# Kernel optimization log

Hardware: AMD Instinct MI355X
Metric: run time of the kernel (lower is better)

The kernel has to match this reference:

```python
import jax, jax.numpy as jnp
import numpy as np

N, D = 8192, 1024
NUM_CLASSES = 128
PPC = 4  # prototypes per class
P = NUM_CLASSES * PPC
ALPHA = 1.0
EPS = 1e-9


def setup_inputs() -> dict:
    key = jax.random.key(0)
    k1, k2, k3 = jax.random.split(key, 3)
    x = jax.random.normal(k1, (N, D), dtype=jnp.float32)
    y = jax.random.randint(k2, (N,), 0, NUM_CLASSES, dtype=jnp.int64)
    prototypes = jax.random.normal(k3, (P, D), dtype=jnp.float32)
    return {"x": x, "y": y, "t_value": 1, "prototypes": prototypes}


def reference(x, y, t_value, prototypes):
    # prototype labels: i // PPC
    proto_labels = jnp.arange(P, dtype=y.dtype) // PPC  # [P]

    x_sq = jnp.sum(x * x, axis=1, keepdims=True)          # [N,1]
    p_sq = jnp.sum(prototypes * prototypes, axis=1)       # [P]
    dist = x_sq + p_sq[None, :] - 2.0 * (x @ prototypes.T)  # [N,P]

    correct_mask = proto_labels[None, :] == y[:, None]    # [N,P]
    inf = jnp.array(jnp.inf, dtype=dist.dtype)
    d1 = jnp.min(jnp.where(correct_mask, dist, inf), axis=1)   # [N]
    d2 = jnp.min(jnp.where(correct_mask, inf, dist), axis=1)   # [N]

    mu = (d1 - d2) / (d1 + d2 + EPS)
    alpha = jnp.log(1.0 + jnp.asarray(t_value, dtype=dist.dtype)) / ALPHA
    return jnp.mean(jax.nn.sigmoid(alpha * mu))
```

## Files before the change

kernel.cpp:

```cpp
#include <hip/hip_runtime.h>
#include <hip/hip_bf16.h>
#include <math.h>
#include <stdint.h>

#define NS 8192
#define DD 1024
#define NP 512
#define NPARTS 8
#define EPSF 1e-9f
#define BIGF 3.0e38f

typedef __attribute__((ext_vector_type(8))) short bf16x8;
typedef __attribute__((ext_vector_type(4))) float f32x4;

__device__ inline unsigned short f32_to_bf16(float f) {
    uint32_t u = __builtin_bit_cast(uint32_t, f);
    uint32_t r = (u + 0x7FFFu + ((u >> 16) & 1u)) >> 16;
    return (unsigned short)r;
}

__global__ __launch_bounds__(256) void prep_kernel(
    const float* __restrict__ x, const float* __restrict__ protos,
    unsigned short* __restrict__ xb, unsigned short* __restrict__ pb,
    float* __restrict__ xsq, float* __restrict__ psq)
{
    int row = blockIdx.x;
    const float* src;
    unsigned short* dstb;
    float* dsts;
    if (row < NS) {
        src = x + (size_t)row * DD; dstb = xb + (size_t)row * DD; dsts = xsq + row;
    } else {
        int r = row - NS;
        src = protos + (size_t)r * DD; dstb = pb + (size_t)r * DD; dsts = psq + r;
    }
    int t = threadIdx.x;
    float4 v = ((const float4*)src)[t];
    float ss = v.x * v.x + v.y * v.y + v.z * v.z + v.w * v.w;
    ushort4 o;
    o.x = f32_to_bf16(v.x); o.y = f32_to_bf16(v.y);
    o.z = f32_to_bf16(v.z); o.w = f32_to_bf16(v.w);
    ((ushort4*)dstb)[t] = o;
    for (int off = 32; off; off >>= 1) ss += __shfl_down(ss, off);
    __shared__ float red[4];
    if ((t & 63) == 0) red[t >> 6] = ss;
    __syncthreads();
    if (t == 0) dsts[0] = red[0] + red[1] + red[2] + red[3];
}

__global__ __launch_bounds__(256) void glvq_gemm(
    const unsigned short* __restrict__ Xb, const unsigned short* __restrict__ Pb,
    const float* __restrict__ xsq, const float* __restrict__ psq,
    const int* __restrict__ y,
    float* __restrict__ d1p, float* __restrict__ d2p)
{
    __shared__ unsigned short As[2][64 * 64];
    __shared__ unsigned short Bs[2][128 * 64];

    const int tid  = threadIdx.x;
    const int lane = tid & 63;
    const int wid  = tid >> 6;
    const int wr = wid >> 1, wc = wid & 1;

    const int d    = blockIdx.x;
    const int xcd  = d & 7;
    const int slot = d >> 3;
    const int mb   = xcd * 16 + (slot & 15);
    const int nb   = slot >> 4;
    const int m0   = mb * 64;
    const int n0   = nb * 128;

    const int srow   = lane >> 3;
    const int scol16 = (lane & 7) ^ srow;
    const int sub = lane & 15, g = lane >> 4;

    f32x4 acc[2][4] = {};

    auto stage = [&](int buf, int kt) {
        const int k0 = kt * 64;
#pragma unroll
        for (int j = 0; j < 2; ++j) {
            const int c = wid * 2 + j;
            const unsigned short* ga = Xb + (size_t)(m0 + c * 8 + srow) * DD + k0 + scol16 * 8;
            __builtin_amdgcn_global_load_lds(
                (const __attribute__((address_space(1))) void*)ga,
                (__attribute__((address_space(3))) void*)((char*)&As[buf][0] + c * 1024), 16, 0, 0);
        }
#pragma unroll
        for (int j = 0; j < 4; ++j) {
            const int c = wid * 4 + j;
            const unsigned short* gb = Pb + (size_t)(n0 + c * 8 + srow) * DD + k0 + scol16 * 8;
            __builtin_amdgcn_global_load_lds(
                (const __attribute__((address_space(1))) void*)gb,
                (__attribute__((address_space(3))) void*)((char*)&Bs[buf][0] + c * 1024), 16, 0, 0);
        }
    };

    auto compute = [&](int buf) {
#pragma unroll
        for (int kk = 0; kk < 2; ++kk) {
            bf16x8 a[2], b[4];
#pragma unroll
            for (int m = 0; m < 2; ++m) {
                const int row = wr * 32 + m * 16 + sub;
                const int c16 = (kk * 4 + g) ^ (row & 7);
                a[m] = *(const bf16x8*)((const char*)&As[buf][0] + row * 128 + c16 * 16);
            }
#pragma unroll
            for (int n = 0; n < 4; ++n) {
                const int row = wc * 64 + n * 16 + sub;
                const int c16 = (kk * 4 + g) ^ (row & 7);
                b[n] = *(const bf16x8*)((const char*)&Bs[buf][0] + row * 128 + c16 * 16);
            }
#pragma unroll
            for (int m = 0; m < 2; ++m)
#pragma unroll
                for (int n = 0; n < 4; ++n)
                    acc[m][n] = __builtin_amdgcn_mfma_f32_16x16x32_bf16(a[m], b[n], acc[m][n], 0, 0, 0);
        }
    };

    stage(0, 0);
    __syncthreads();
    int cur = 0;
#pragma unroll 1
    for (int kt = 0; kt < DD / 64 - 1; ++kt) {
        stage(cur ^ 1, kt + 1);
        compute(cur);
        __syncthreads();
        cur ^= 1;
    }
    compute(cur);

    float psqv[4];
    int   lab[4];
#pragma unroll
    for (int n = 0; n < 4; ++n) {
        const int col = n0 + wc * 64 + n * 16 + sub;
        psqv[n] = psq[col];
        lab[n]  = col >> 2;
    }
    const int part = nb * 2 + wc;
#pragma unroll
    for (int m = 0; m < 2; ++m) {
#pragma unroll
        for (int r = 0; r < 4; ++r) {
            const int row = m0 + wr * 32 + m * 16 + g * 4 + r;
            const float xs = xsq[row];
            const int yy = y[row];
            float d1 = BIGF, d2 = BIGF;
#pragma unroll
            for (int n = 0; n < 4; ++n) {
                const float dist = xs + psqv[n] - 2.0f * acc[m][n][r];
                if (lab[n] == yy) d1 = fminf(d1, dist);
                else              d2 = fminf(d2, dist);
            }
            for (int off = 8; off; off >>= 1) {
                d1 = fminf(d1, __shfl_xor(d1, off));
                d2 = fminf(d2, __shfl_xor(d2, off));
            }
            if (sub == 0) {
                d1p[part * NS + row] = d1;
                d2p[part * NS + row] = d2;
            }
        }
    }
}

__global__ __launch_bounds__(256) void finalize_kernel(
    const float* __restrict__ d1p, const float* __restrict__ d2p,
    const int* __restrict__ tval, float* __restrict__ bsum)
{
    const int row = blockIdx.x * 256 + threadIdx.x;
    float d1 = BIGF, d2 = BIGF;
#pragma unroll
    for (int p = 0; p < NPARTS; ++p) {
        d1 = fminf(d1, d1p[p * NS + row]);
        d2 = fminf(d2, d2p[p * NS + row]);
    }
    const float mu = (d1 - d2) / (d1 + d2 + EPSF);
    const float alpha = logf(1.0f + (float)tval[0]);
    float s = 1.0f / (1.0f + expf(-alpha * mu));
    for (int off = 32; off; off >>= 1) s += __shfl_down(s, off);
    __shared__ float red[4];
    if ((threadIdx.x & 63) == 0) red[threadIdx.x >> 6] = s;
    __syncthreads();
    if (threadIdx.x == 0) bsum[blockIdx.x] = red[0] + red[1] + red[2] + red[3];
}

__global__ void final_sum(const float* __restrict__ bsum, float* __restrict__ out) {
    float s = (threadIdx.x < NS / 256) ? bsum[threadIdx.x] : 0.0f;
    for (int off = 32; off; off >>= 1) s += __shfl_down(s, off);
    if (threadIdx.x == 0) out[0] = s * (1.0f / (float)NS);
}

extern "C" void kernel_launch(void* const* d_in, const int* in_sizes, int n_in,
                              void* d_out, int out_size, void* d_ws, size_t ws_size,
                              hipStream_t stream) {
    const float* x      = (const float*)d_in[0];
    const int*   y      = (const int*)d_in[1];
    const int*   tval   = (const int*)d_in[2];
    const float* protos = (const float*)d_in[3];
    float* out = (float*)d_out;

    char* ws = (char*)d_ws;
    unsigned short* xb  = (unsigned short*)(ws);
    unsigned short* pb  = (unsigned short*)(ws + (size_t)NS * DD * 2);
    float* xsq  = (float*)(ws + (size_t)(NS + NP) * DD * 2);
    float* psq  = (float*)(ws + (size_t)(NS + NP) * DD * 2 + NS * 4);
    float* d1p  = (float*)(ws + (size_t)(NS + NP) * DD * 2 + (NS + NP) * 4);
    float* d2p  = d1p + (size_t)NPARTS * NS;
    float* bsum = d2p + (size_t)NPARTS * NS;

    prep_kernel<<<NS + NP, 256, 0, stream>>>(x, protos, xb, pb, xsq, psq);
    glvq_gemm<<<(NS / 64) * (NP / 128), 256, 0, stream>>>(xb, pb, xsq, psq, y, d1p, d2p);
    finalize_kernel<<<NS / 256, 256, 0, stream>>>(d1p, d2p, tval, bsum);
    final_sum<<<1, 64, 0, stream>>>(bsum, out);
}
```

Baseline: 37.41 us.

## Fuse x bf16 conversion and row norms into GEMM A-tile staging

The separate pass that converts x to bf16 and computes its row squared norms is removed. The GEMM kernel now loads fp32 x directly into registers, converts it with packed bf16 conversion instructions, writes it to swizzled LDS, and accumulates the row norms along the way. The goal is to avoid writing and re-reading a 16 MB bf16 copy of x and to save a kernel launch. The cost is that each x tile is read in fp32 by all four N-blocks, which doubles A-side traffic per block, and the A loads now pass through registers instead of async global-to-LDS copies, which adds register pressure and latency to the main loop.

After: 39.59 us. 1.06x slower.

```diff
diff --git a/kernel.cpp b/kernel.cpp
--- a/kernel.cpp
+++ b/kernel.cpp
@@ -6,6 +6,9 @@
 #define NS 8192
 #define DD 1024
 #define NP 512
+#define BK 64
+#define MT 64
+#define NT 128
 #define NPARTS 8
 #define EPSF 1e-9f
 #define BIGF 3.0e38f
@@ -19,98 +22,113 @@
     return (unsigned short)r;
 }
 
-__global__ __launch_bounds__(256) void prep_kernel(
-    const float* __restrict__ x, const float* __restrict__ protos,
-    unsigned short* __restrict__ xb, unsigned short* __restrict__ pb,
-    float* __restrict__ xsq, float* __restrict__ psq)
+__device__ inline uint32_t cvt_pk(float lo, float hi) {
+    uint32_t r;
+    asm("v_cvt_pk_bf16_f32 %0, %1, %2" : "=v"(r) : "v"(lo), "v"(hi));
+    return r;
+}
+
+__global__ __launch_bounds__(256) void prep_protos(
+    const float* __restrict__ protos,
+    unsigned short* __restrict__ pb, float* __restrict__ psq)
 {
-    int row = blockIdx.x;
-    const float* src;
-    unsigned short* dstb;
-    float* dsts;
-    if (row < NS) {
-        src = x + (size_t)row * DD; dstb = xb + (size_t)row * DD; dsts = xsq + row;
-    } else {
-        int r = row - NS;
-        src = protos + (size_t)r * DD; dstb = pb + (size_t)r * DD; dsts = psq + r;
-    }
-    int t = threadIdx.x;
-    float4 v = ((const float4*)src)[t];
+    const int row = blockIdx.x;
+    const int t = threadIdx.x;
+    float4 v = ((const float4*)(protos + (size_t)row * DD))[t];
     float ss = v.x * v.x + v.y * v.y + v.z * v.z + v.w * v.w;
     ushort4 o;
     o.x = f32_to_bf16(v.x); o.y = f32_to_bf16(v.y);
     o.z = f32_to_bf16(v.z); o.w = f32_to_bf16(v.w);
-    ((ushort4*)dstb)[t] = o;
+    ((ushort4*)(pb + (size_t)row * DD))[t] = o;
     for (int off = 32; off; off >>= 1) ss += __shfl_down(ss, off);
     __shared__ float red[4];
     if ((t & 63) == 0) red[t >> 6] = ss;
     __syncthreads();
-    if (t == 0) dsts[0] = red[0] + red[1] + red[2] + red[3];
-}
-
-__global__ __launch_bounds__(256) void glvq_gemm(
-    const unsigned short* __restrict__ Xb, const unsigned short* __restrict__ Pb,
-    const float* __restrict__ xsq, const float* __restrict__ psq,
-    const int* __restrict__ y,
+    if (t == 0) psq[row] = red[0] + red[1] + red[2] + red[3];
+}
+
+__global__ __launch_bounds__(256) void glvq_fused(
+    const float* __restrict__ x, const unsigned short* __restrict__ pb,
+    const float* __restrict__ psq, const int* __restrict__ y,
     float* __restrict__ d1p, float* __restrict__ d2p)
 {
-    __shared__ unsigned short As[2][64 * 64];
-    __shared__ unsigned short Bs[2][128 * 64];
+    __shared__ unsigned short As[2][MT * BK];
+    __shared__ unsigned short Bs[2][NT * BK];
+    __shared__ float xs_l[MT];
 
     const int tid  = threadIdx.x;
     const int lane = tid & 63;
     const int wid  = tid >> 6;
-    const int wr = wid >> 1, wc = wid & 1;
-
+    const int wr = wid >> 1;
+    const int wc = wid & 1;
     const int d    = blockIdx.x;
     const int xcd  = d & 7;
     const int slot = d >> 3;
     const int mb   = xcd * 16 + (slot & 15);
     const int nb   = slot >> 4;
-    const int m0   = mb * 64;
-    const int n0   = nb * 128;
+    const int m0   = mb * MT;
+    const int n0   = nb * NT;
 
     const int srow   = lane >> 3;
     const int scol16 = (lane & 7) ^ srow;
     const int sub = lane & 15, g = lane >> 4;
 
+    const int arow = tid >> 2;
+    const int acb  = (tid & 3) * 2;
+    const float* xrow = x + (size_t)(m0 + arow) * DD;
+
     f32x4 acc[2][4] = {};
-
-    auto stage = [&](int buf, int kt) {
-        const int k0 = kt * 64;
-#pragma unroll
-        for (int j = 0; j < 2; ++j) {
-            const int c = wid * 2 + j;
-            const unsigned short* ga = Xb + (size_t)(m0 + c * 8 + srow) * DD + k0 + scol16 * 8;
-            __builtin_amdgcn_global_load_lds(
-                (const __attribute__((address_space(1))) void*)ga,
-                (__attribute__((address_space(3))) void*)((char*)&As[buf][0] + c * 1024), 16, 0, 0);
-        }
+    float xss = 0.0f;
+    float4 av[4];
+
+    auto stageB = [&](int buf, int kt) {
+        const int k0 = kt * BK;
 #pragma unroll
         for (int j = 0; j < 4; ++j) {
             const int c = wid * 4 + j;
-            const unsigned short* gb = Pb + (size_t)(n0 + c * 8 + srow) * DD + k0 + scol16 * 8;
+            const unsigned short* gb = pb + (size_t)(n0 + c * 8 + srow) * DD + k0 + scol16 * 8;
             __builtin_amdgcn_global_load_lds(
                 (const __attribute__((address_space(1))) void*)gb,
-                (__attribute__((address_space(3))) void*)((char*)&Bs[buf][0] + c * 1024), 16, 0, 0);
-        }
-    };
-
+                (__attribute__((address_space(3))) void*)((char*)&Bs[buf][0] + c * 1024),
+                16, 0, 0);
+        }
+    };
+    auto loadA = [&](int kt) {
+#pragma unroll
+        for (int j = 0; j < 2; ++j) {
+            const float* p = xrow + kt * BK + (acb + j) * 8;
+            av[2 * j]     = *(const float4*)(p);
+            av[2 * j + 1] = *(const float4*)(p + 4);
+        }
+    };
+    auto writeA = [&](int buf) {
+#pragma unroll
+        for (int j = 0; j < 2; ++j) {
+            float4 u = av[2 * j], w = av[2 * j + 1];
+            xss += u.x * u.x + u.y * u.y + u.z * u.z + u.w * u.w
+                 + w.x * w.x + w.y * w.y + w.z * w.z + w.w * w.w;
+            uint4 o;
+            o.x = cvt_pk(u.x, u.y); o.y = cvt_pk(u.z, u.w);
+            o.z = cvt_pk(w.x, w.y); o.w = cvt_pk(w.z, w.w);
+            const int c = acb + j;
+            *(uint4*)((char*)&As[buf][0] + arow * 128 + ((c ^ (arow & 7)) * 16)) = o;
+        }
+    };
     auto compute = [&](int buf) {
 #pragma unroll
         for (int kk = 0; kk < 2; ++kk) {
             bf16x8 a[2], b[4];
 #pragma unroll
             for (int m = 0; m < 2; ++m) {
-                const int row = wr * 32 + m * 16 + sub;
-                const int c16 = (kk * 4 + g) ^ (row & 7);
-                a[m] = *(const bf16x8*)((const char*)&As[buf][0] + row * 128 + c16 * 16);
+                const int rowa = wr * 32 + m * 16 + sub;
+                const int c16 = (kk * 4 + g) ^ (rowa & 7);
+                a[m] = *(const bf16x8*)((const char*)&As[buf][0] + rowa * 128 + c16 * 16);
             }
 #pragma unroll
             for (int n = 0; n < 4; ++n) {
-                const int row = wc * 64 + n * 16 + sub;
-                const int c16 = (kk * 4 + g) ^ (row & 7);
-                b[n] = *(const bf16x8*)((const char*)&Bs[buf][0] + row * 128 + c16 * 16);
+                const int rowb = wc * 64 + n * 16 + sub;
+                const int c16 = (kk * 4 + g) ^ (rowb & 7);
+                b[n] = *(const bf16x8*)((const char*)&Bs[buf][0] + rowb * 128 + c16 * 16);
             }
 #pragma unroll
             for (int m = 0; m < 2; ++m)
@@ -120,17 +138,25 @@
         }
     };
 
-    stage(0, 0);
-    __syncthreads();
+    loadA(0); stageB(0, 0); writeA(0);
+    __syncthreads();
+
     int cur = 0;
 #pragma unroll 1
-    for (int kt = 0; kt < DD / 64 - 1; ++kt) {
-        stage(cur ^ 1, kt + 1);
+    for (int kt = 0; kt < DD / BK - 1; ++kt) {
+        stageB(cur ^ 1, kt + 1);
+        loadA(kt + 1);
         compute(cur);
+        writeA(cur ^ 1);
         __syncthreads();
         cur ^= 1;
     }
     compute(cur);
+
+    xss += __shfl_xor(xss, 1);
+    xss += __shfl_xor(xss, 2);
+    if ((tid & 3) == 0) xs_l[arow] = xss;
+    __syncthreads();
 
     float psqv[4];
     int   lab[4];
@@ -145,9 +171,9 @@
     for (int m = 0; m < 2; ++m) {
 #pragma unroll
         for (int r = 0; r < 4; ++r) {
-            const int row = m0 + wr * 32 + m * 16 + g * 4 + r;
-            const float xs = xsq[row];
-            const int yy = y[row];
+            const int rl = wr * 32 + m * 16 + g * 4 + r;
+            const float xs = xs_l[rl];
+            const int yy = y[m0 + rl];
             float d1 = BIGF, d2 = BIGF;
 #pragma unroll
             for (int n = 0; n < 4; ++n) {
@@ -160,8 +186,8 @@
                 d2 = fminf(d2, __shfl_xor(d2, off));
             }
             if (sub == 0) {
-                d1p[part * NS + row] = d1;
-                d2p[part * NS + row] = d2;
+                d1p[part * NS + m0 + rl] = d1;
+                d2p[part * NS + m0 + rl] = d2;
             }
         }
     }
@@ -204,16 +230,14 @@
     float* out = (float*)d_out;
 
     char* ws = (char*)d_ws;
-    unsigned short* xb  = (unsigned short*)(ws);
-    unsigned short* pb  = (unsigned short*)(ws + (size_t)NS * DD * 2);
-    float* xsq  = (float*)(ws + (size_t)(NS + NP) * DD * 2);
-    float* psq  = (float*)(ws + (size_t)(NS + NP) * DD * 2 + NS * 4);
-    float* d1p  = (float*)(ws + (size_t)(NS + NP) * DD * 2 + (NS + NP) * 4);
+    unsigned short* pb = (unsigned short*)(ws);
+    float* psq  = (float*)(ws + (size_t)NP * DD * 2);
+    float* d1p  = psq + NP;
     float* d2p  = d1p + (size_t)NPARTS * NS;
     float* bsum = d2p + (size_t)NPARTS * NS;
 
-    prep_kernel<<<NS + NP, 256, 0, stream>>>(x, protos, xb, pb, xsq, psq);
-    glvq_gemm<<<(NS / 64) * (NP / 128), 256, 0, stream>>>(xb, pb, xsq, psq, y, d1p, d2p);
+    prep_protos<<<NP, 256, 0, stream>>>(protos, pb, psq);
+    glvq_fused<<<(NS / MT) * (NP / NT), 256, 0, stream>>>(x, pb, psq, y, d1p, d2p);
     finalize_kernel<<<NS / 256, 256, 0, stream>>>(d1p, d2p, tval, bsum);
     final_sum<<<1, 64, 0, stream>>>(bsum, out);
 }
```

## Triple-buffer GEMM K-loop with vmcnt waits, single barrier, and setprio

Applied to the files above, without the earlier changes.

Moves the bf16 GEMM main loop from double to triple buffering in LDS. It keeps two tiles in flight, waits with s_waitcnt vmcnt(6) and one raw barrier per step instead of __syncthreads after compute, and raises wave priority around the MFMA section. The aim is to hide global-to-LDS load latency better and remove one barrier wait per iteration. In exchange it uses more LDS (72KB per block), which may limit occupancy, and relies on hand-counted vmcnt correctness.

New measurement: 37.42 us. Within noise of the previous version (+0.0%).

```diff
diff --git a/kernel.cpp b/kernel.cpp
--- a/kernel.cpp
+++ b/kernel.cpp
@@ -6,6 +6,10 @@
 #define NS 8192
 #define DD 1024
 #define NP 512
+#define BK 64
+#define MT 64
+#define NT 128
+#define NSTEP (DD / BK)
 #define NPARTS 8
 #define EPSF 1e-9f
 #define BIGF 3.0e38f
@@ -48,27 +52,27 @@
     if (t == 0) dsts[0] = red[0] + red[1] + red[2] + red[3];
 }
 
-__global__ __launch_bounds__(256) void glvq_gemm(
-    const unsigned short* __restrict__ Xb, const unsigned short* __restrict__ Pb,
+__global__ __launch_bounds__(256, 2) void glvq_gemm(
+    const unsigned short* __restrict__ xb, const unsigned short* __restrict__ pb,
     const float* __restrict__ xsq, const float* __restrict__ psq,
     const int* __restrict__ y,
     float* __restrict__ d1p, float* __restrict__ d2p)
 {
-    __shared__ unsigned short As[2][64 * 64];
-    __shared__ unsigned short Bs[2][128 * 64];
+    __shared__ unsigned short As[3][MT * BK];
+    __shared__ unsigned short Bs[3][NT * BK];
 
     const int tid  = threadIdx.x;
     const int lane = tid & 63;
     const int wid  = tid >> 6;
-    const int wr = wid >> 1, wc = wid & 1;
-
+    const int wr = wid >> 1;
+    const int wc = wid & 1;
     const int d    = blockIdx.x;
     const int xcd  = d & 7;
     const int slot = d >> 3;
     const int mb   = xcd * 16 + (slot & 15);
     const int nb   = slot >> 4;
-    const int m0   = mb * 64;
-    const int n0   = nb * 128;
+    const int m0   = mb * MT;
+    const int n0   = nb * NT;
 
     const int srow   = lane >> 3;
     const int scol16 = (lane & 7) ^ srow;
@@ -77,22 +81,24 @@
     f32x4 acc[2][4] = {};
 
     auto stage = [&](int buf, int kt) {
-        const int k0 = kt * 64;
+        const int k0 = kt * BK;
 #pragma unroll
         for (int j = 0; j < 2; ++j) {
             const int c = wid * 2 + j;
-            const unsigned short* ga = Xb + (size_t)(m0 + c * 8 + srow) * DD + k0 + scol16 * 8;
+            const unsigned short* ga = xb + (size_t)(m0 + c * 8 + srow) * DD + k0 + scol16 * 8;
             __builtin_amdgcn_global_load_lds(
                 (const __attribute__((address_space(1))) void*)ga,
-                (__attribute__((address_space(3))) void*)((char*)&As[buf][0] + c * 1024), 16, 0, 0);
+                (__attribute__((address_space(3))) void*)((char*)&As[buf][0] + c * 1024),
+                16, 0, 0);
         }
 #pragma unroll
         for (int j = 0; j < 4; ++j) {
             const int c = wid * 4 + j;
-            const unsigned short* gb = Pb + (size_t)(n0 + c * 8 + srow) * DD + k0 + scol16 * 8;
+            const unsigned short* gb = pb + (size_t)(n0 + c * 8 + srow) * DD + k0 + scol16 * 8;
             __builtin_amdgcn_global_load_lds(
                 (const __attribute__((address_space(1))) void*)gb,
-                (__attribute__((address_space(3))) void*)((char*)&Bs[buf][0] + c * 1024), 16, 0, 0);
+                (__attribute__((address_space(3))) void*)((char*)&Bs[buf][0] + c * 1024),
+                16, 0, 0);
         }
     };
 
@@ -102,15 +108,15 @@
             bf16x8 a[2], b[4];
 #pragma unroll
             for (int m = 0; m < 2; ++m) {
-                const int row = wr * 32 + m * 16 + sub;
-                const int c16 = (kk * 4 + g) ^ (row & 7);
-                a[m] = *(const bf16x8*)((const char*)&As[buf][0] + row * 128 + c16 * 16);
+                const int rowa = wr * 32 + m * 16 + sub;
+                const int c16 = (kk * 4 + g) ^ (rowa & 7);
+                a[m] = *(const bf16x8*)((const char*)&As[buf][0] + rowa * 128 + c16 * 16);
             }
 #pragma unroll
             for (int n = 0; n < 4; ++n) {
-                const int row = wc * 64 + n * 16 + sub;
-                const int c16 = (kk * 4 + g) ^ (row & 7);
-                b[n] = *(const bf16x8*)((const char*)&Bs[buf][0] + row * 128 + c16 * 16);
+                const int rowb = wc * 64 + n * 16 + sub;
+                const int c16 = (kk * 4 + g) ^ (rowb & 7);
+                b[n] = *(const bf16x8*)((const char*)&Bs[buf][0] + rowb * 128 + c16 * 16);
             }
 #pragma unroll
             for (int m = 0; m < 2; ++m)
@@ -121,16 +127,29 @@
     };
 
     stage(0, 0);
-    __syncthreads();
-    int cur = 0;
+    stage(1, 1);
+
+    int cb = 0, sb = 2;
 #pragma unroll 1
-    for (int kt = 0; kt < DD / 64 - 1; ++kt) {
-        stage(cur ^ 1, kt + 1);
-        compute(cur);
-        __syncthreads();
-        cur ^= 1;
-    }
-    compute(cur);
+    for (int kt = 0; kt < NSTEP - 2; ++kt) {
+        asm volatile("s_waitcnt vmcnt(6)" ::: "memory");
+        __builtin_amdgcn_s_barrier();
+        stage(sb, kt + 2);
+        __builtin_amdgcn_s_setprio(1);
+        compute(cb);
+        __builtin_amdgcn_s_setprio(0);
+        cb = (cb == 2) ? 0 : cb + 1;
+        sb = (sb == 2) ? 0 : sb + 1;
+    }
+    asm volatile("s_waitcnt vmcnt(6)" ::: "memory");
+    __builtin_amdgcn_s_barrier();
+    __builtin_amdgcn_s_setprio(1);
+    compute(cb);
+    __builtin_amdgcn_s_setprio(0);
+    cb = (cb == 2) ? 0 : cb + 1;
+    asm volatile("s_waitcnt vmcnt(0)" ::: "memory");
+    __builtin_amdgcn_s_barrier();
+    compute(cb);
 
     float psqv[4];
     int   lab[4];
@@ -145,9 +164,9 @@
     for (int m = 0; m < 2; ++m) {
 #pragma unroll
         for (int r = 0; r < 4; ++r) {
-            const int row = m0 + wr * 32 + m * 16 + g * 4 + r;
-            const float xs = xsq[row];
-            const int yy = y[row];
+            const int rl = wr * 32 + m * 16 + g * 4 + r;
+            const float xs = xsq[m0 + rl];
+            const int yy = y[m0 + rl];
             float d1 = BIGF, d2 = BIGF;
 #pragma unroll
             for (int n = 0; n < 4; ++n) {
@@ -160,8 +179,8 @@
                 d2 = fminf(d2, __shfl_xor(d2, off));
             }
             if (sub == 0) {
-                d1p[part * NS + row] = d1;
-                d2p[part * NS + row] = d2;
+                d1p[part * NS + m0 + rl] = d1;
+                d2p[part * NS + m0 + rl] = d2;
             }
         }
     }
@@ -204,8 +223,8 @@
     float* out = (float*)d_out;
 
     char* ws = (char*)d_ws;
-    unsigned short* xb  = (unsigned short*)(ws);
-    unsigned short* pb  = (unsigned short*)(ws + (size_t)NS * DD * 2);
+    unsigned short* xb = (unsigned short*)(ws);
+    unsigned short* pb = (unsigned short*)(ws + (size_t)NS * DD * 2);
     float* xsq  = (float*)(ws + (size_t)(NS + NP) * DD * 2);
     float* psq  = (float*)(ws + (size_t)(NS + NP) * DD * 2 + NS * 4);
     float* d1p  = (float*)(ws + (size_t)(NS + NP) * DD * 2 + (NS + NP) * 4);
@@ -213,7 +232,7 @@
     float* bsum = d2p + (size_t)NPARTS * NS;
 
     prep_kernel<<<NS + NP, 256, 0, stream>>>(x, protos, xb, pb, xsq, psq);
-    glvq_gemm<<<(NS / 64) * (NP / 128), 256, 0, stream>>>(xb, pb, xsq, psq, y, d1p, d2p);
+    glvq_gemm<<<(NS / MT) * (NP / NT), 256, 0, stream>>>(xb, pb, xsq, psq, y, d1p, d2p);
     finalize_kernel<<<NS / 256, 256, 0, stream>>>(d1p, d2p, tval, bsum);
     final_sum<<<1, 64, 0, stream>>>(bsum, out);
 }
```
